# Optimization experiments

Hardware: AMD Instinct MI355X
Metric: run time of the kernel (lower is better)

## Reference

```python
import jax, jax.numpy as jnp
import numpy as np

D_MODEL = 1024
D_STATE = 128
HEADDIM = 64
EXPAND = 2
CHUNK = 64
D_CONV = 4
D_INNER = EXPAND * D_MODEL          # 2048
NHEADS = D_INNER // HEADDIM         # 32
D_IN_PROJ = 2 * D_INNER + 2 * D_STATE + NHEADS  # 4384
CONV_CH = D_INNER + 2 * D_STATE     # 2304
EPS = 1e-5


def segsum(x):
    # x: (..., T) -> (..., T, T); out[i, j] = sum_{k=j+1..i} x[k] for i>=j else -inf
    T = x.shape[-1]
    m1 = jnp.tril(jnp.ones((T, T), bool), -1)
    xr = jnp.where(m1, x[..., :, None], 0.0)   # zero above/at diagonal before cumsum
    s = jnp.cumsum(xr, axis=-2)
    m0 = jnp.tril(jnp.ones((T, T), bool), 0)
    return jnp.where(m0, s, -jnp.inf)


def ssd(x, A, B, C, chunk):
    # x: (b, L, h, p); A: (b, L, h); B, C: (b, L, n)  (the h=1 dim of the torch code is squeezed)
    b, L, h, p = x.shape
    c = L // chunk
    x = x.reshape(b, c, chunk, h, p)
    A = A.reshape(b, c, chunk, h).transpose(0, 3, 1, 2)  # (b, h, c, l)
    B = B.reshape(b, c, chunk, -1)                       # (b, c, l, n)
    C = C.reshape(b, c, chunk, -1)
    A_cum = jnp.cumsum(A, axis=-1)                       # (b, h, c, l)
    Lm = jnp.exp(segsum(A))                              # (b, h, c, l, l)
    # intra-chunk (diagonal block) output
    Y_diag = jnp.einsum('bcln,bcsn,bhcls,bcshp->bclhp', C, B, Lm, x)
    # per-chunk states
    decay_states = jnp.exp(A_cum[:, :, :, -1:] - A_cum)  # (b, h, c, l)
    states = jnp.einsum('bcln,bhcl,bclhp->bchpn', B, decay_states, x)
    init = jnp.zeros_like(states[:, :1])
    states = jnp.concatenate([init, states], axis=1)     # (b, c+1, h, p, n)
    # inter-chunk recurrence
    Ac_last = jnp.pad(A_cum[:, :, :, -1], ((0, 0), (0, 0), (1, 0)))  # (b, h, c+1)
    decay_chunk = jnp.exp(segsum(Ac_last))               # (b, h, c+1, c+1)
    new_states = jnp.einsum('bhzc,bchpn->bzhpn', decay_chunk, states)
    states = new_states[:, :-1]                          # (b, c, h, p, n)
    sdo = jnp.exp(A_cum)
    Y_off = jnp.einsum('bcln,bchpn,bhcl->bclhp', C, states, sdo)
    return (Y_diag + Y_off).reshape(b, L, h, p)


def setup_inputs() -> dict:
    key = jax.random.key(0)
    ks = jax.random.split(key, 8)
    return {
        'u': jax.random.normal(ks[0], (2, 4096, D_MODEL), jnp.float32),
        'W_in': jax.random.normal(ks[1], (D_MODEL, D_IN_PROJ), jnp.float32) * 0.02,
        'conv_w': jax.random.normal(ks[2], (CONV_CH, D_CONV), jnp.float32) * 0.3,
        'conv_b': jax.random.normal(ks[3], (CONV_CH,), jnp.float32) * 0.1,
        'dt_bias': jax.random.normal(ks[4], (NHEADS,), jnp.float32),
        'A_log': jax.random.normal(ks[5], (NHEADS,), jnp.float32) * 0.5,
        'D': jax.random.normal(ks[6], (NHEADS,), jnp.float32),
        'norm_w': jnp.ones((D_INNER,), jnp.float32),
        'W_out': jax.random.normal(ks[7], (D_INNER, D_MODEL), jnp.float32) * 0.02,
    }


def reference(u, W_in, conv_w, conv_b, dt_bias, A_log, D, norm_w, W_out):
    b, L, _ = u.shape
    zxbcdt = u @ W_in                                    # (b, L, 4384)
    z = zxbcdt[..., :D_INNER]
    xBC = zxbcdt[..., D_INNER:D_INNER + CONV_CH]
    dt = jax.nn.softplus(zxbcdt[..., -NHEADS:] + dt_bias)  # (b, L, h)
    # depthwise causal conv (Conv1d pad=d_conv-1, truncated to L == left-pad only)
    xc = jnp.pad(xBC.transpose(0, 2, 1), ((0, 0), (0, 0), (D_CONV - 1, 0)))
    xc = jax.lax.conv_general_dilated(
        xc, conv_w[:, None, :], (1,), 'VALID',
        feature_group_count=CONV_CH,
        dimension_numbers=('NCH', 'OIH', 'NCH')) + conv_b[None, :, None]
    xBC = jax.nn.silu(xc.transpose(0, 2, 1))             # (b, L, 2304)
    x = xBC[..., :D_INNER].reshape(b, L, NHEADS, HEADDIM)
    B = xBC[..., D_INNER:D_INNER + D_STATE]
    C = xBC[..., D_INNER + D_STATE:]
    A = -jnp.exp(A_log)                                  # (h,)
    y = ssd(x * dt[..., None], A * dt, B, C, CHUNK)
    y = y + x * D[:, None]
    y = y.reshape(b, L, D_INNER)
    # RMSNorm with gate z
    y = y * jax.nn.silu(z)
    y = y * jax.lax.rsqrt(jnp.mean(y * y, axis=-1, keepdims=True) + EPS) * norm_w
    return y @ W_out
```

## Files before the change

### kernel.cpp

```cpp
#include <hip/hip_runtime.h>
#include <hip/hip_bf16.h>
#include <math.h>

#define D_MODEL   1024
#define D_STATE   128
#define HEADDIM   64
#define CHUNK     64
#define D_INNER   2048
#define NHEADS    32
#define D_IN_PROJ 4384
#define CONV_CH   2304
#define RCOLS     2336
#define WINT_ROWS 4480
#define BATCH     2
#define SEQ       4096
#define NCHUNK    64
#define ROWS      (BATCH*SEQ)
#define EPS_RMS   1e-5f

typedef __hip_bfloat16 bf16;
typedef __bf16 bf16x8_t __attribute__((ext_vector_type(8)));
typedef float  f32x4_t  __attribute__((ext_vector_type(4)));

__device__ __forceinline__ float siluf_(float x){ return x/(1.f+expf(-x)); }
__device__ __forceinline__ float ldf(const float* p){ return *p; }
__device__ __forceinline__ float ldf(const bf16* p){ return __bfloat162float(*p); }
__device__ __forceinline__ void  stf(float* p, float v){ *p = v; }
__device__ __forceinline__ void  stf(bf16* p, float v){ *p = __float2bfloat16(v); }

__device__ __forceinline__ __bf16 tobf(float v){
    __hip_bfloat16 t = __float2bfloat16(v);
    return *reinterpret_cast<__bf16*>(&t);
}
__device__ __forceinline__ unsigned short bfbits(float v){
    __hip_bfloat16 t = __float2bfloat16(v);
    return *reinterpret_cast<unsigned short*>(&t);
}
__device__ __forceinline__ float bfbits2f(unsigned short u){
    union { unsigned u; float f; } cv; cv.u = ((unsigned)u) << 16; return cv.f;
}

__device__ __forceinline__ void async16(const void* g, void* l) {
    __builtin_amdgcn_global_load_lds(
        (const __attribute__((address_space(1))) unsigned int*)g,
        (__attribute__((address_space(3))) unsigned int*)l, 16, 0, 0);
}

struct GemmCore {
    f32x4_t acc[4][4];
    __device__ __forceinline__ void run(const bf16* __restrict__ A, int lda,
                                        const bf16* __restrict__ Bt, int ldb,
                                        int row0, int col0, int k0, int k1,
                                        __bf16* As, __bf16* Bs,
                                        int wave, int lane) {
        const int quad = lane >> 4, l16 = lane & 15;
        const int wr = (wave >> 1) * 64, wc = (wave & 1) * 64;
#pragma unroll
        for (int i = 0; i < 4; ++i)
#pragma unroll
            for (int j = 0; j < 4; ++j) acc[i][j] = (f32x4_t){0.f, 0.f, 0.f, 0.f};
        const int ca0 = wave * 2, ca1 = wave * 2 + 1;
        const int srow = lane >> 2, scol = (lane & 3) * 8;
        const bf16* Ag0 = A  + (size_t)(row0 + ca0 * 16 + srow) * lda + scol;
        const bf16* Ag1 = A  + (size_t)(row0 + ca1 * 16 + srow) * lda + scol;
        const bf16* Bg0 = Bt + (size_t)(col0 + ca0 * 16 + srow) * ldb + scol;
        const bf16* Bg1 = Bt + (size_t)(col0 + ca1 * 16 + srow) * ldb + scol;
        __bf16* Al0 = As + ca0 * 512;
        __bf16* Al1 = As + ca1 * 512;
        __bf16* Bl0 = Bs + ca0 * 512;
        __bf16* Bl1 = Bs + ca1 * 512;
        for (int kk = k0; kk < k1; kk += 32) {
            async16(Ag0 + kk, Al0);
            async16(Ag1 + kk, Al1);
            async16(Bg0 + kk, Bl0);
            async16(Bg1 + kk, Bl1);
            __syncthreads();
            bf16x8_t af[4], bfr[4];
#pragma unroll
            for (int mi = 0; mi < 4; ++mi)
                af[mi] = *(const bf16x8_t*)(As + (wr + mi * 16 + l16) * 32 + quad * 8);
#pragma unroll
            for (int ni = 0; ni < 4; ++ni)
                bfr[ni] = *(const bf16x8_t*)(Bs + (wc + ni * 16 + l16) * 32 + quad * 8);
#pragma unroll
            for (int mi = 0; mi < 4; ++mi)
#pragma unroll
                for (int ni = 0; ni < 4; ++ni)
                    acc[mi][ni] = __builtin_amdgcn_mfma_f32_16x16x32_bf16(
                        af[mi], bfr[ni], acc[mi][ni], 0, 0, 0);
            __syncthreads();
        }
    }
};

__global__ __launch_bounds__(256) void gemm_zr_fused(const bf16* __restrict__ A,
                                                     const bf16* __restrict__ Bt,
                                                     bf16* __restrict__ Z,
                                                     bf16* __restrict__ R) {
    __shared__ __align__(16) __bf16 As[128 * 32];
    __shared__ __align__(16) __bf16 Bs[128 * 32];
    const int tid = threadIdx.x, wave = tid >> 6, lane = tid & 63;
    const int quad = lane >> 4, l16 = lane & 15;
    const int row0 = blockIdx.x * 128;
    const int ct   = blockIdx.y;
    GemmCore g;
    g.run(A, D_MODEL, Bt, D_MODEL, row0, ct * 128, 0, D_MODEL, As, Bs, wave, lane);

    bf16* Cp; int ldc_, cl0, ncols;
    if (ct < 16) { Cp = Z; ldc_ = D_INNER; cl0 = ct * 128;          ncols = D_INNER; }
    else         { Cp = R; ldc_ = RCOLS;   cl0 = ct * 128 - D_INNER; ncols = RCOLS; }
    const int wr = (wave >> 1) * 64, wc = (wave & 1) * 64;
#pragma unroll
    for (int ni = 0; ni < 4; ++ni) {
        int gc = cl0 + wc + ni * 16 + l16;
        if (gc >= ncols) continue;
#pragma unroll
        for (int mi = 0; mi < 4; ++mi)
#pragma unroll
            for (int r = 0; r < 4; ++r) {
                int gr = row0 + wr + mi * 16 + quad * 4 + r;
                stf(&Cp[(size_t)gr * ldc_ + gc], g.acc[mi][ni][r]);
            }
    }
}

__global__ __launch_bounds__(256) void gemm_out_kernel(const bf16* __restrict__ A,
                                                       const bf16* __restrict__ Bt,
                                                       float* __restrict__ out) {
    __shared__ __align__(16) __bf16 As[128 * 32];
    __shared__ __align__(16) __bf16 Bs[128 * 32];
    const int tid = threadIdx.x, wave = tid >> 6, lane = tid & 63;
    const int quad = lane >> 4, l16 = lane & 15;
    const int row0 = blockIdx.x * 128;
    const int col0 = blockIdx.y * 128;
    GemmCore g;
    g.run(A, D_INNER, Bt, D_INNER, row0, col0, 0, D_INNER, As, Bs, wave, lane);
    const int wr = (wave >> 1) * 64, wc = (wave & 1) * 64;
#pragma unroll
    for (int ni = 0; ni < 4; ++ni) {
        int gc = col0 + wc + ni * 16 + l16;
#pragma unroll
        for (int mi = 0; mi < 4; ++mi)
#pragma unroll
            for (int r = 0; r < 4; ++r) {
                int gr = row0 + wr + mi * 16 + quad * 4 + r;
                out[(size_t)gr * D_MODEL + gc] = g.acc[mi][ni][r];
            }
    }
}

__global__ void cvt_bf16_kernel(const float* __restrict__ src,
                                bf16* __restrict__ dst, int n4) {
    int i = blockIdx.x * 256 + threadIdx.x;
    if (i >= n4) return;
    float4 v = ((const float4*)src)[i];
    dst[i * 4 + 0] = __float2bfloat16(v.x);
    dst[i * 4 + 1] = __float2bfloat16(v.y);
    dst[i * 4 + 2] = __float2bfloat16(v.z);
    dst[i * 4 + 3] = __float2bfloat16(v.w);
}

__global__ __launch_bounds__(256) void transpose_cvt_kernel(const float* __restrict__ W,
                                                            bf16* __restrict__ Wt,
                                                            int R, int C, int Cpad) {
    __shared__ float tile[32][33];
    int c0 = blockIdx.x * 32, r0 = blockIdx.y * 32;
    int tx = threadIdx.x & 31, ty = threadIdx.x >> 5;
    for (int i = ty; i < 32; i += 8) {
        int r = r0 + i, c = c0 + tx;
        tile[i][tx] = (c < C) ? W[(size_t)r * C + c] : 0.f;
    }
    __syncthreads();
    for (int i = ty; i < 32; i += 8) {
        int c = c0 + i, r = r0 + tx;
        stf(&Wt[(size_t)c * R + r], tile[tx][i]);
    }
}

__global__ void prep_convw_kernel(const float* __restrict__ conv_w,
                                  bf16* __restrict__ Wc) {
    int i = blockIdx.x * 256 + threadIdx.x;
    if (i >= CONV_CH * 4) return;
    int ch = i >> 2, k = i & 3;
    Wc[k * CONV_CH + ch] = __float2bfloat16(conv_w[ch * 4 + k]);
}

__global__ __launch_bounds__(256) void conv_silu_kernel(const bf16* __restrict__ R,
                                                        const bf16* __restrict__ Wc,
                                                        const float* __restrict__ conv_b,
                                                        bf16* __restrict__ xBC) {
    int idx = blockIdx.x * 256 + threadIdx.x;
    int rq = idx / 288;
    int g = idx - rq * 288;
    int ch0 = g * 8;
    int row0 = rq * 4;
    int l0 = row0 & (SEQ - 1);

    uint4 rv[7];
#pragma unroll
    for (int j = 0; j < 7; ++j) {
        int ls = l0 - 3 + j;
        rv[j] = (ls >= 0) ? *(const uint4*)&R[(size_t)(row0 - 3 + j) * RCOLS + ch0]
                          : make_uint4(0u, 0u, 0u, 0u);
    }
    uint4 wv[4];
#pragma unroll
    for (int k = 0; k < 4; ++k)
        wv[k] = *(const uint4*)&Wc[k * CONV_CH + ch0];
    float4 b0 = ((const float4*)conv_b)[ch0 / 4];
    float4 b1 = ((const float4*)conv_b)[ch0 / 4 + 1];
    const float bias[8] = {b0.x, b0.y, b0.z, b0.w, b1.x, b1.y, b1.z, b1.w};
    float wf[4][8];
#pragma unroll
    for (int k = 0; k < 4; ++k) {
        const unsigned* wp = (const unsigned*)&wv[k];
#pragma unroll
        for (int j2 = 0; j2 < 4; ++j2) {
            wf[k][2 * j2]     = bfbits2f((unsigned short)(wp[j2] & 0xffff));
            wf[k][2 * j2 + 1] = bfbits2f((unsigned short)(wp[j2] >> 16));
        }
    }
#pragma unroll
    for (int j = 0; j < 4; ++j) {
        float acc[8];
#pragma unroll
        for (int cc = 0; cc < 8; ++cc) acc[cc] = bias[cc];
#pragma unroll
        for (int k = 0; k < 4; ++k) {
            const unsigned* vp = (const unsigned*)&rv[j + k];
#pragma unroll
            for (int j2 = 0; j2 < 4; ++j2) {
                unsigned v = vp[j2];
                acc[2 * j2]     += wf[k][2 * j2]     * bfbits2f((unsigned short)(v & 0xffff));
                acc[2 * j2 + 1] += wf[k][2 * j2 + 1] * bfbits2f((unsigned short)(v >> 16));
            }
        }
        unsigned o[4];
#pragma unroll
        for (int j2 = 0; j2 < 4; ++j2)
            o[j2] = (unsigned)bfbits(siluf_(acc[2 * j2])) |
                    ((unsigned)bfbits(siluf_(acc[2 * j2 + 1])) << 16);
        *(uint4*)&xBC[(size_t)(row0 + j) * CONV_CH + ch0] = make_uint4(o[0], o[1], o[2], o[3]);
    }
}

__global__ void dt_kernel(const bf16* __restrict__ R,
                          const float* __restrict__ dt_bias,
                          float* __restrict__ dtb) {
    int i = blockIdx.x * 256 + threadIdx.x;
    int row = i >> 2, h0 = (i & 3) * 8;
    uint4 v = *(const uint4*)&R[(size_t)row * RCOLS + CONV_CH + h0];
    float4 bia0 = ((const float4*)dt_bias)[h0 / 4];
    float4 bia1 = ((const float4*)dt_bias)[h0 / 4 + 1];
    const unsigned vv[4] = {v.x, v.y, v.z, v.w};
    const float bb[8] = {bia0.x, bia0.y, bia0.z, bia0.w, bia1.x, bia1.y, bia1.z, bia1.w};
    float o[8];
#pragma unroll
    for (int j = 0; j < 4; ++j) {
        float a = bfbits2f((unsigned short)(vv[j] & 0xffff)) + bb[2*j];
        float c = bfbits2f((unsigned short)(vv[j] >> 16)) + bb[2*j+1];
        o[2*j]   = (a > 20.f) ? a : log1pf(expf(a));
        o[2*j+1] = (c > 20.f) ? c : log1pf(expf(c));
    }
    float* dp = &dtb[(size_t)row * NHEADS + h0];
    *(float4*)dp       = make_float4(o[0], o[1], o[2], o[3]);
    *(float4*)(dp + 4) = make_float4(o[4], o[5], o[6], o[7]);
}

__global__ void acum_kernel(const float* __restrict__ dtb,
                            const float* __restrict__ A_log,
                            float* __restrict__ Acum) {
    int bch = blockIdx.x;
    int h = bch & 31;
    int bc = bch >> 5;
    int c = bc & 63, b = bc >> 6;
    int row0 = b * SEQ + c * CHUNK;
    __shared__ float sh[64];
    int l = threadIdx.x;
    float Ah = -expf(A_log[h]);
    sh[l] = Ah * dtb[(size_t)(row0 + l) * NHEADS + h];
    __syncthreads();
    float s = 0.f;
    for (int j = 0; j <= l; ++j) s += sh[j];
    Acum[(size_t)bch * 64 + l] = s;
}

__global__ __launch_bounds__(256) void states_mfma_kernel(const bf16* __restrict__ xBC,
                                                          const float* __restrict__ dtb,
                                                          const float* __restrict__ Acum,
                                                          bf16* __restrict__ states) {
    __shared__ __align__(16) __bf16 BsT[128 * 72];
    __shared__ __align__(16) __bf16 xdT[4][64 * 72];
    __shared__ float dtdec[4][64];
    int bcq = blockIdx.x;
    int hq = bcq & 7, bc = bcq >> 3;
    int c = bc & 63, b = bc >> 6;
    int tid = threadIdx.x, wave = tid >> 6, lane = tid & 63;
    int h = hq * 4 + wave;
    int bch = bc * 32 + h;
    int row0 = b * SEQ + c * CHUNK;
    int quad = lane >> 4, l16 = lane & 15;

    {
        float alast = Acum[(size_t)bch * 64 + 63];
        float a = Acum[(size_t)bch * 64 + lane];
        dtdec[wave][lane] = dtb[(size_t)(row0 + lane) * NHEADS + h] * expf(alast - a);
    }
    __syncthreads();
    for (int it = 0; it < 16; ++it) {
        int i2 = tid + 256 * it;
        int l = i2 >> 6;
        int n0 = (i2 & 63) * 2;
        unsigned v = *(const unsigned*)&xBC[(size_t)(row0 + l) * CONV_CH + D_INNER + n0];
        *(unsigned short*)&BsT[(n0    ) * 72 + l] = (unsigned short)(v & 0xffff);
        *(unsigned short*)&BsT[(n0 + 1) * 72 + l] = (unsigned short)(v >> 16);
    }
    for (int it = 0; it < 32; ++it) {
        int l = 2 * it + (lane >> 5);
        int p0 = (lane & 31) * 2;
        unsigned v = *(const unsigned*)&xBC[(size_t)(row0 + l) * CONV_CH + h * 64 + p0];
        float f = dtdec[wave][l];
        xdT[wave][(p0    ) * 72 + l] = tobf(bfbits2f((unsigned short)(v & 0xffff)) * f);
        xdT[wave][(p0 + 1) * 72 + l] = tobf(bfbits2f((unsigned short)(v >> 16)) * f);
    }
    __syncthreads();

    f32x4_t acc[4][8];
#pragma unroll
    for (int i = 0; i < 4; ++i)
#pragma unroll
        for (int j = 0; j < 8; ++j) acc[i][j] = (f32x4_t){0.f, 0.f, 0.f, 0.f};
#pragma unroll
    for (int ks = 0; ks < 2; ++ks) {
        bf16x8_t a[4], bb[8];
#pragma unroll
        for (int mi = 0; mi < 4; ++mi)
            a[mi] = *(const bf16x8_t*)(&xdT[wave][(mi * 16 + l16) * 72 + ks * 32 + quad * 8]);
#pragma unroll
        for (int ni = 0; ni < 8; ++ni)
            bb[ni] = *(const bf16x8_t*)(&BsT[(ni * 16 + l16) * 72 + ks * 32 + quad * 8]);
#pragma unroll
        for (int mi = 0; mi < 4; ++mi)
#pragma unroll
            for (int ni = 0; ni < 8; ++ni)
                acc[mi][ni] = __builtin_amdgcn_mfma_f32_16x16x32_bf16(
                    a[mi], bb[ni], acc[mi][ni], 0, 0, 0);
    }
#pragma unroll
    for (int ni = 0; ni < 8; ++ni) {
        int n = ni * 16 + l16;
#pragma unroll
        for (int mi = 0; mi < 4; ++mi)
#pragma unroll
            for (int r = 0; r < 4; ++r) {
                int p = mi * 16 + quad * 4 + r;
                stf(&states[(size_t)bch * 8192 + p * 128 + n], acc[mi][ni][r]);
            }
    }
}

__global__ void scan_kernel(const float* __restrict__ Acum,
                            bf16* __restrict__ states) {
    int i = blockIdx.x * 256 + threadIdx.x;
    int pn0 = (i & 2047) * 4;
    int bh = i >> 11;
    int h = bh & 31, b = bh >> 5;
    float carry[4] = {0.f, 0.f, 0.f, 0.f};
    for (int c = 0; c < NCHUNK; ++c) {
        int bch = (b * NCHUNK + c) * NHEADS + h;
        bf16* sp = &states[(size_t)bch * 8192 + pn0];
        uint2 v = *(const uint2*)sp;
        float s0 = bfbits2f((unsigned short)(v.x & 0xffff));
        float s1 = bfbits2f((unsigned short)(v.x >> 16));
        float s2 = bfbits2f((unsigned short)(v.y & 0xffff));
        float s3 = bfbits2f((unsigned short)(v.y >> 16));
        uint2 o;
        o.x = (unsigned)bfbits(carry[0]) | ((unsigned)bfbits(carry[1]) << 16);
        o.y = (unsigned)bfbits(carry[2]) | ((unsigned)bfbits(carry[3]) << 16);
        *(uint2*)sp = o;
        float dec = expf(Acum[(size_t)bch * 64 + 63]);
        carry[0] = carry[0] * dec + s0;
        carry[1] = carry[1] * dec + s1;
        carry[2] = carry[2] * dec + s2;
        carry[3] = carry[3] * dec + s3;
    }
}

__global__ __launch_bounds__(64) void y_mfma_kernel(const bf16* __restrict__ xBC,
                                                    const float* __restrict__ dtb,
                                                    const float* __restrict__ Acum,
                                                    const bf16* __restrict__ states,
                                                    const float* __restrict__ Dv,
                                                    bf16* __restrict__ y) {
    __shared__ __align__(16) __bf16 Mm[64 * 72];
    __shared__ __align__(16) __bf16 xsT[64 * 72];
    __shared__ float acs[64], dtss[64], sdos[64];
    int bch = blockIdx.x;
    int h = bch & 31, bc = bch >> 5;
    int c = bc & 63, b = bc >> 6;
    int row0 = b * SEQ + c * CHUNK;
    int lane = threadIdx.x;
    int quad = lane >> 4, l16 = lane & 15;

    {
        float a = Acum[(size_t)bch * 64 + lane];
        acs[lane] = a;
        sdos[lane] = expf(a);
        dtss[lane] = dtb[(size_t)(row0 + lane) * NHEADS + h];
    }
    for (int it = 0; it < 32; ++it) {
        int l = 2 * it + (lane >> 5);
        int p0 = (lane & 31) * 2;
        unsigned v = *(const unsigned*)&xBC[(size_t)(row0 + l) * CONV_CH + h * 64 + p0];
        *(unsigned short*)&xsT[(p0    ) * 72 + l] = (unsigned short)(v & 0xffff);
        *(unsigned short*)&xsT[(p0 + 1) * 72 + l] = (unsigned short)(v >> 16);
    }
    __syncthreads();

    f32x4_t gacc[4][4];
#pragma unroll
    for (int i = 0; i < 4; ++i)
#pragma unroll
        for (int j = 0; j < 4; ++j) gacc[i][j] = (f32x4_t){0.f, 0.f, 0.f, 0.f};
#pragma unroll
    for (int ks = 0; ks < 4; ++ks) {
        bf16x8_t a[4], bb[4];
#pragma unroll
        for (int mi = 0; mi < 4; ++mi)
            a[mi] = *(const bf16x8_t*)&xBC[(size_t)(row0 + mi * 16 + l16) * CONV_CH +
                                           D_INNER + D_STATE + ks * 32 + quad * 8];
#pragma unroll
        for (int ni = 0; ni < 4; ++ni)
            bb[ni] = *(const bf16x8_t*)&xBC[(size_t)(row0 + ni * 16 + l16) * CONV_CH +
                                            D_INNER + ks * 32 + quad * 8];
#pragma unroll
        for (int mi = 0; mi < 4; ++mi)
#pragma unroll
            for (int ni = 0; ni <= mi; ++ni)
                gacc[mi][ni] = __builtin_amdgcn_mfma_f32_16x16x32_bf16(
                    a[mi], bb[ni], gacc[mi][ni], 0, 0, 0);
    }
#pragma unroll
    for (int ni = 0; ni < 4; ++ni) {
        int s = ni * 16 + l16;
        float ds = dtss[s], as = acs[s];
#pragma unroll
        for (int mi = 0; mi < 4; ++mi)
#pragma unroll
            for (int r = 0; r < 4; ++r) {
                int l = mi * 16 + quad * 4 + r;
                float coef = (s <= l) ? gacc[mi][ni][r] * ds * expf(acs[l] - as) : 0.f;
                Mm[l * 72 + s] = tobf(coef);
            }
    }
    __syncthreads();

    f32x4_t acc[4][4];
#pragma unroll
    for (int i = 0; i < 4; ++i)
#pragma unroll
        for (int j = 0; j < 4; ++j) acc[i][j] = (f32x4_t){0.f, 0.f, 0.f, 0.f};

#pragma unroll
    for (int ks = 0; ks < 2; ++ks) {
        bf16x8_t a[4], bb[4];
#pragma unroll
        for (int mi = 0; mi < 4; ++mi)
            a[mi] = *(const bf16x8_t*)(&Mm[(mi * 16 + l16) * 72 + ks * 32 + quad * 8]);
#pragma unroll
        for (int ni = 0; ni < 4; ++ni)
            bb[ni] = *(const bf16x8_t*)(&xsT[(ni * 16 + l16) * 72 + ks * 32 + quad * 8]);
#pragma unroll
        for (int mi = 0; mi < 4; ++mi)
#pragma unroll
            for (int ni = 0; ni < 4; ++ni)
                acc[mi][ni] = __builtin_amdgcn_mfma_f32_16x16x32_bf16(
                    a[mi], bb[ni], acc[mi][ni], 0, 0, 0);
    }
    float sdo_mi[4];
#pragma unroll
    for (int mi = 0; mi < 4; ++mi) sdo_mi[mi] = sdos[mi * 16 + l16];
#pragma unroll
    for (int ks = 0; ks < 4; ++ks) {
        bf16x8_t a[4], bb[4];
#pragma unroll
        for (int mi = 0; mi < 4; ++mi) {
            const unsigned* cp = (const unsigned*)&xBC[(size_t)(row0 + mi * 16 + l16) * CONV_CH
                                                       + D_INNER + D_STATE + ks * 32 + quad * 8];
            float sc = sdo_mi[mi];
#pragma unroll
            for (int jj = 0; jj < 4; ++jj) {
                unsigned v = cp[jj];
                a[mi][2 * jj    ] = tobf(bfbits2f((unsigned short)(v & 0xffff)) * sc);
                a[mi][2 * jj + 1] = tobf(bfbits2f((unsigned short)(v >> 16)) * sc);
            }
        }
#pragma unroll
        for (int ni = 0; ni < 4; ++ni)
            bb[ni] = *(const bf16x8_t*)&states[(size_t)bch * 8192 + (ni * 16 + l16) * 128
                                               + ks * 32 + quad * 8];
#pragma unroll
        for (int mi = 0; mi < 4; ++mi)
#pragma unroll
            for (int ni = 0; ni < 4; ++ni)
                acc[mi][ni] = __builtin_amdgcn_mfma_f32_16x16x32_bf16(
                    a[mi], bb[ni], acc[mi][ni], 0, 0, 0);
    }
    float Dh = Dv[h];
#pragma unroll
    for (int ni = 0; ni < 4; ++ni) {
        int p = ni * 16 + l16;
#pragma unroll
        for (int mi = 0; mi < 4; ++mi)
#pragma unroll
            for (int r = 0; r < 4; ++r) {
                int l = mi * 16 + quad * 4 + r;
                float xv = bfbits2f(*(const unsigned short*)&xsT[p * 72 + l]);
                stf(&y[(size_t)(row0 + l) * D_INNER + h * 64 + p],
                    acc[mi][ni][r] + Dh * xv);
            }
    }
}

__global__ __launch_bounds__(256) void gate_norm_kernel(const bf16* __restrict__ Z,
                                                        const float* __restrict__ nw,
                                                        bf16* __restrict__ y) {
    int row = blockIdx.x;
    int tid = threadIdx.x;
    int col0 = tid * 8;
    uint4 zv = *(const uint4*)&Z[(size_t)row * D_INNER + col0];
    uint4 yv = *(const uint4*)&y[(size_t)row * D_INNER + col0];
    const unsigned zz[4] = {zv.x, zv.y, zv.z, zv.w};
    const unsigned yy[4] = {yv.x, yv.y, yv.z, yv.w};
    float vals[8];
    float local = 0.f;
#pragma unroll
    for (int j = 0; j < 4; ++j) {
        float z0 = bfbits2f((unsigned short)(zz[j] & 0xffff));
        float z1 = bfbits2f((unsigned short)(zz[j] >> 16));
        float y0 = bfbits2f((unsigned short)(yy[j] & 0xffff));
        float y1 = bfbits2f((unsigned short)(yy[j] >> 16));
        float v0 = y0 * siluf_(z0);
        float v1 = y1 * siluf_(z1);
        vals[2*j] = v0; vals[2*j+1] = v1;
        local += v0 * v0 + v1 * v1;
    }
#pragma unroll
    for (int off = 32; off; off >>= 1) local += __shfl_down(local, off, 64);
    __shared__ float wsum[4];
    if ((tid & 63) == 0) wsum[tid >> 6] = local;
    __syncthreads();
    float total = wsum[0] + wsum[1] + wsum[2] + wsum[3];
    float scale = rsqrtf(total / (float)D_INNER + EPS_RMS);
    float4 w0 = ((const float4*)nw)[col0 / 4];
    float4 w1 = ((const float4*)nw)[col0 / 4 + 1];
    const float ww[8] = {w0.x, w0.y, w0.z, w0.w, w1.x, w1.y, w1.z, w1.w};
    unsigned o[4];
#pragma unroll
    for (int j = 0; j < 4; ++j)
        o[j] = (unsigned)bfbits(vals[2*j] * scale * ww[2*j]) |
               ((unsigned)bfbits(vals[2*j+1] * scale * ww[2*j+1]) << 16);
    *(uint4*)&y[(size_t)row * D_INNER + col0] = make_uint4(o[0], o[1], o[2], o[3]);
}

extern "C" void kernel_launch(void* const* d_in, const int* in_sizes, int n_in,
                              void* d_out, int out_size, void* d_ws, size_t ws_size,
                              hipStream_t stream) {
    const float* u       = (const float*)d_in[0];
    const float* W_in    = (const float*)d_in[1];
    const float* conv_w  = (const float*)d_in[2];
    const float* conv_b  = (const float*)d_in[3];
    const float* dt_bias = (const float*)d_in[4];
    const float* A_log   = (const float*)d_in[5];
    const float* Dv      = (const float*)d_in[6];
    const float* norm_w  = (const float*)d_in[7];
    const float* W_out   = (const float*)d_in[8];
    float* out = (float*)d_out;

    const size_t sz_xBC    = (size_t)ROWS * CONV_CH * 2;
    const size_t sz_Z      = (size_t)ROWS * D_INNER * 2;
    const size_t sz_y      = (size_t)ROWS * D_INNER * 2;
    const size_t sz_states = (size_t)BATCH * NCHUNK * NHEADS * 8192 * 2;
    const size_t sz_dtb    = (size_t)ROWS * NHEADS * 4;
    const size_t sz_Acum   = (size_t)BATCH * NCHUNK * NHEADS * 64 * 4;
    const size_t sz_WinT   = (size_t)WINT_ROWS * D_MODEL * 2;
    const size_t sz_WoutT  = (size_t)D_MODEL * D_INNER * 2;
    const size_t sz_Wc     = (size_t)CONV_CH * 4 * 2;
    const size_t need = sz_xBC + sz_Z + sz_y + sz_states + sz_dtb + sz_Acum +
                        sz_WinT + sz_WoutT + sz_Wc;
    if (ws_size < need) {
        hipMemsetAsync(d_out, 0, (size_t)out_size * sizeof(float), stream);
        return;
    }
    char* ws = (char*)d_ws;
    size_t off = 0;
    bf16*  xBC    = (bf16*) (ws + off); off += sz_xBC;
    bf16*  Z      = (bf16*) (ws + off); off += sz_Z;
    bf16*  y      = (bf16*) (ws + off); off += sz_y;
    bf16*  states = (bf16*) (ws + off); off += sz_states;
    float* dtb    = (float*)(ws + off); off += sz_dtb;
    float* Acum   = (float*)(ws + off); off += sz_Acum;
    bf16*  W_inT  = (bf16*) (ws + off); off += sz_WinT;
    bf16*  W_outT = (bf16*) (ws + off); off += sz_WoutT;
    bf16*  Wc     = (bf16*) (ws + off); off += sz_Wc;
    bf16*  R        = states;
    bf16*  u_bf16   = (bf16*)((char*)states + (size_t)ROWS * RCOLS * 2);

    cvt_bf16_kernel<<<(ROWS * D_MODEL / 4 + 255) / 256, 256, 0, stream>>>(
        u, u_bf16, ROWS * D_MODEL / 4);
    transpose_cvt_kernel<<<dim3(WINT_ROWS / 32, D_MODEL / 32), 256, 0, stream>>>(
        W_in, W_inT, D_MODEL, D_IN_PROJ, WINT_ROWS);
    transpose_cvt_kernel<<<dim3(D_MODEL / 32, D_INNER / 32), 256, 0, stream>>>(
        W_out, W_outT, D_INNER, D_MODEL, D_MODEL);
    prep_convw_kernel<<<(CONV_CH * 4 + 255) / 256, 256, 0, stream>>>(conv_w, Wc);
    gemm_zr_fused<<<dim3(ROWS / 128, 35), 256, 0, stream>>>(u_bf16, W_inT, Z, R);
    conv_silu_kernel<<<ROWS / 4 * 288 / 256, 256, 0, stream>>>(R, Wc, conv_b, xBC);
    dt_kernel<<<ROWS * 4 / 256, 256, 0, stream>>>(R, dt_bias, dtb);
    acum_kernel<<<BATCH * NCHUNK * NHEADS, 64, 0, stream>>>(dtb, A_log, Acum);
    states_mfma_kernel<<<BATCH * NCHUNK * 8, 256, 0, stream>>>(xBC, dtb, Acum, states);
    scan_kernel<<<BATCH * NHEADS * 2048 / 256, 256, 0, stream>>>(Acum, states);
    y_mfma_kernel<<<BATCH * NCHUNK * NHEADS, 64, 0, stream>>>(
        xBC, dtb, Acum, states, Dv, y);
    gate_norm_kernel<<<ROWS, 256, 0, stream>>>(Z, norm_w, y);
    gemm_out_kernel<<<dim3(ROWS / 128, D_MODEL / 128), 256, 0, stream>>>(
        y, W_outT, out);
}
```

Measured before the change: 415.0 us.

## Fuse prep kernels, precompute chunk decays, prefetch scan loads, pack LDS transposes

Measured after the change: 411.5 us. About the same (-0.8%).

```diff
diff --git a/kernel.cpp b/kernel.cpp
--- a/kernel.cpp
+++ b/kernel.cpp
@@ -23,8 +23,6 @@
 typedef float  f32x4_t  __attribute__((ext_vector_type(4)));
 
 __device__ __forceinline__ float siluf_(float x){ return x/(1.f+expf(-x)); }
-__device__ __forceinline__ float ldf(const float* p){ return *p; }
-__device__ __forceinline__ float ldf(const bf16* p){ return __bfloat162float(*p); }
 __device__ __forceinline__ void  stf(float* p, float v){ *p = v; }
 __device__ __forceinline__ void  stf(bf16* p, float v){ *p = __float2bfloat16(v); }
 
@@ -149,40 +147,58 @@
     }
 }
 
-__global__ void cvt_bf16_kernel(const float* __restrict__ src,
-                                bf16* __restrict__ dst, int n4) {
-    int i = blockIdx.x * 256 + threadIdx.x;
-    if (i >= n4) return;
-    float4 v = ((const float4*)src)[i];
-    dst[i * 4 + 0] = __float2bfloat16(v.x);
-    dst[i * 4 + 1] = __float2bfloat16(v.y);
-    dst[i * 4 + 2] = __float2bfloat16(v.z);
-    dst[i * 4 + 3] = __float2bfloat16(v.w);
-}
-
-__global__ __launch_bounds__(256) void transpose_cvt_kernel(const float* __restrict__ W,
-                                                            bf16* __restrict__ Wt,
-                                                            int R, int C, int Cpad) {
+__global__ __launch_bounds__(256) void prep_all_kernel(const float* __restrict__ u,
+                                                       bf16* __restrict__ u_bf16,
+                                                       const float* __restrict__ W_in,
+                                                       bf16* __restrict__ W_inT,
+                                                       const float* __restrict__ W_out,
+                                                       bf16* __restrict__ W_outT,
+                                                       const float* __restrict__ conv_w,
+                                                       bf16* __restrict__ Wc) {
     __shared__ float tile[32][33];
-    int c0 = blockIdx.x * 32, r0 = blockIdx.y * 32;
-    int tx = threadIdx.x & 31, ty = threadIdx.x >> 5;
-    for (int i = ty; i < 32; i += 8) {
-        int r = r0 + i, c = c0 + tx;
-        tile[i][tx] = (c < C) ? W[(size_t)r * C + c] : 0.f;
-    }
-    __syncthreads();
-    for (int i = ty; i < 32; i += 8) {
-        int c = c0 + i, r = r0 + tx;
-        stf(&Wt[(size_t)c * R + r], tile[tx][i]);
-    }
-}
-
-__global__ void prep_convw_kernel(const float* __restrict__ conv_w,
-                                  bf16* __restrict__ Wc) {
-    int i = blockIdx.x * 256 + threadIdx.x;
-    if (i >= CONV_CH * 4) return;
-    int ch = i >> 2, k = i & 3;
-    Wc[k * CONV_CH + ch] = __float2bfloat16(conv_w[ch * 4 + k]);
+    int bid = blockIdx.x;
+    const int tid = threadIdx.x;
+
+    auto do_transpose = [&](const float* W, bf16* Wt, int R, int C, int c0, int r0) {
+        int tx = tid & 31, ty = tid >> 5;
+        for (int i = ty; i < 32; i += 8) {
+            int r = r0 + i, c = c0 + tx;
+            tile[i][tx] = (c < C) ? W[(size_t)r * C + c] : 0.f;
+        }
+        __syncthreads();
+        for (int i = ty; i < 32; i += 8) {
+            int c = c0 + i, r = r0 + tx;
+            stf(&Wt[(size_t)c * R + r], tile[tx][i]);
+        }
+    };
+
+    if (bid < 8192) {
+        int i = bid * 256 + tid;
+        float4 v = ((const float4*)u)[i];
+        u_bf16[i * 4 + 0] = __float2bfloat16(v.x);
+        u_bf16[i * 4 + 1] = __float2bfloat16(v.y);
+        u_bf16[i * 4 + 2] = __float2bfloat16(v.z);
+        u_bf16[i * 4 + 3] = __float2bfloat16(v.w);
+        return;
+    }
+    bid -= 8192;
+    if (bid < (WINT_ROWS / 32) * (D_MODEL / 32)) {
+        int bx = bid % (WINT_ROWS / 32), by = bid / (WINT_ROWS / 32);
+        do_transpose(W_in, W_inT, D_MODEL, D_IN_PROJ, bx * 32, by * 32);
+        return;
+    }
+    bid -= (WINT_ROWS / 32) * (D_MODEL / 32);
+    if (bid < (D_MODEL / 32) * (D_INNER / 32)) {
+        int bx = bid % (D_MODEL / 32), by = bid / (D_MODEL / 32);
+        do_transpose(W_out, W_outT, D_INNER, D_MODEL, bx * 32, by * 32);
+        return;
+    }
+    bid -= (D_MODEL / 32) * (D_INNER / 32);
+    int i = bid * 256 + tid;
+    if (i < CONV_CH * 4) {
+        int ch = i >> 2, k = i & 3;
+        Wc[k * CONV_CH + ch] = __float2bfloat16(conv_w[ch * 4 + k]);
+    }
 }
 
 __global__ __launch_bounds__(256) void conv_silu_kernel(const bf16* __restrict__ R,
@@ -269,7 +285,8 @@
 
 __global__ void acum_kernel(const float* __restrict__ dtb,
                             const float* __restrict__ A_log,
-                            float* __restrict__ Acum) {
+                            float* __restrict__ Acum,
+                            float* __restrict__ decs) {
     int bch = blockIdx.x;
     int h = bch & 31;
     int bc = bch >> 5;
@@ -283,6 +300,7 @@
     float s = 0.f;
     for (int j = 0; j <= l; ++j) s += sh[j];
     Acum[(size_t)bch * 64 + l] = s;
+    if (l == 63) decs[bch] = expf(s);
 }
 
 __global__ __launch_bounds__(256) void states_mfma_kernel(const bf16* __restrict__ xBC,
@@ -307,21 +325,27 @@
         dtdec[wave][lane] = dtb[(size_t)(row0 + lane) * NHEADS + h] * expf(alast - a);
     }
     __syncthreads();
+    for (int it = 0; it < 8; ++it) {
+        int i2 = tid + 256 * it;
+        int l0 = (i2 >> 6) * 2;
+        int n0 = (i2 & 63) * 2;
+        unsigned v0 = *(const unsigned*)&xBC[(size_t)(row0 + l0    ) * CONV_CH + D_INNER + n0];
+        unsigned v1 = *(const unsigned*)&xBC[(size_t)(row0 + l0 + 1) * CONV_CH + D_INNER + n0];
+        *(unsigned*)&BsT[(n0    ) * 72 + l0] = (v0 & 0xffffu) | (v1 << 16);
+        *(unsigned*)&BsT[(n0 + 1) * 72 + l0] = (v0 >> 16) | (v1 & 0xffff0000u);
+    }
     for (int it = 0; it < 16; ++it) {
-        int i2 = tid + 256 * it;
-        int l = i2 >> 6;
-        int n0 = (i2 & 63) * 2;
-        unsigned v = *(const unsigned*)&xBC[(size_t)(row0 + l) * CONV_CH + D_INNER + n0];
-        *(unsigned short*)&BsT[(n0    ) * 72 + l] = (unsigned short)(v & 0xffff);
-        *(unsigned short*)&BsT[(n0 + 1) * 72 + l] = (unsigned short)(v >> 16);
-    }
-    for (int it = 0; it < 32; ++it) {
-        int l = 2 * it + (lane >> 5);
+        int l0 = 4 * it + ((lane >> 5) << 1);
         int p0 = (lane & 31) * 2;
-        unsigned v = *(const unsigned*)&xBC[(size_t)(row0 + l) * CONV_CH + h * 64 + p0];
-        float f = dtdec[wave][l];
-        xdT[wave][(p0    ) * 72 + l] = tobf(bfbits2f((unsigned short)(v & 0xffff)) * f);
-        xdT[wave][(p0 + 1) * 72 + l] = tobf(bfbits2f((unsigned short)(v >> 16)) * f);
+        unsigned v0 = *(const unsigned*)&xBC[(size_t)(row0 + l0    ) * CONV_CH + h * 64 + p0];
+        unsigned v1 = *(const unsigned*)&xBC[(size_t)(row0 + l0 + 1) * CONV_CH + h * 64 + p0];
+        float f0 = dtdec[wave][l0], f1 = dtdec[wave][l0 + 1];
+        unsigned w0 = (unsigned)bfbits(bfbits2f((unsigned short)(v0 & 0xffff)) * f0)
+                    | ((unsigned)bfbits(bfbits2f((unsigned short)(v1 & 0xffff)) * f1) << 16);
+        unsigned w1 = (unsigned)bfbits(bfbits2f((unsigned short)(v0 >> 16)) * f0)
+                    | ((unsigned)bfbits(bfbits2f((unsigned short)(v1 >> 16)) * f1) << 16);
+        *(unsigned*)&xdT[wave][(p0    ) * 72 + l0] = w0;
+        *(unsigned*)&xdT[wave][(p0 + 1) * 72 + l0] = w1;
     }
     __syncthreads();
 
@@ -359,30 +383,30 @@
     }
 }
 
-__global__ void scan_kernel(const float* __restrict__ Acum,
+__global__ void scan_kernel(const float* __restrict__ decs,
                             bf16* __restrict__ states) {
     int i = blockIdx.x * 256 + threadIdx.x;
     int pn0 = (i & 2047) * 4;
     int bh = i >> 11;
     int h = bh & 31, b = bh >> 5;
+    int bch0 = b * NCHUNK * NHEADS + h;
+    const size_t cstride = (size_t)NHEADS * 8192;
     float carry[4] = {0.f, 0.f, 0.f, 0.f};
+    bf16* sp = &states[(size_t)bch0 * 8192 + pn0];
+    uint2 v = *(const uint2*)sp;
     for (int c = 0; c < NCHUNK; ++c) {
-        int bch = (b * NCHUNK + c) * NHEADS + h;
-        bf16* sp = &states[(size_t)bch * 8192 + pn0];
-        uint2 v = *(const uint2*)sp;
-        float s0 = bfbits2f((unsigned short)(v.x & 0xffff));
-        float s1 = bfbits2f((unsigned short)(v.x >> 16));
-        float s2 = bfbits2f((unsigned short)(v.y & 0xffff));
-        float s3 = bfbits2f((unsigned short)(v.y >> 16));
+        bf16* spn = sp + ((c + 1 < NCHUNK) ? cstride : 0);
+        uint2 vn = *(const uint2*)spn;
+        float dec = decs[bch0 + c * NHEADS];
         uint2 o;
         o.x = (unsigned)bfbits(carry[0]) | ((unsigned)bfbits(carry[1]) << 16);
         o.y = (unsigned)bfbits(carry[2]) | ((unsigned)bfbits(carry[3]) << 16);
         *(uint2*)sp = o;
-        float dec = expf(Acum[(size_t)bch * 64 + 63]);
-        carry[0] = carry[0] * dec + s0;
-        carry[1] = carry[1] * dec + s1;
-        carry[2] = carry[2] * dec + s2;
-        carry[3] = carry[3] * dec + s3;
+        carry[0] = carry[0] * dec + bfbits2f((unsigned short)(v.x & 0xffff));
+        carry[1] = carry[1] * dec + bfbits2f((unsigned short)(v.x >> 16));
+        carry[2] = carry[2] * dec + bfbits2f((unsigned short)(v.y & 0xffff));
+        carry[3] = carry[3] * dec + bfbits2f((unsigned short)(v.y >> 16));
+        sp = spn; v = vn;
     }
 }
 
@@ -408,12 +432,13 @@
         sdos[lane] = expf(a);
         dtss[lane] = dtb[(size_t)(row0 + lane) * NHEADS + h];
     }
-    for (int it = 0; it < 32; ++it) {
-        int l = 2 * it + (lane >> 5);
+    for (int it = 0; it < 16; ++it) {
+        int l0 = 4 * it + ((lane >> 5) << 1);
         int p0 = (lane & 31) * 2;
-        unsigned v = *(const unsigned*)&xBC[(size_t)(row0 + l) * CONV_CH + h * 64 + p0];
-        *(unsigned short*)&xsT[(p0    ) * 72 + l] = (unsigned short)(v & 0xffff);
-        *(unsigned short*)&xsT[(p0 + 1) * 72 + l] = (unsigned short)(v >> 16);
+        unsigned v0 = *(const unsigned*)&xBC[(size_t)(row0 + l0    ) * CONV_CH + h * 64 + p0];
+        unsigned v1 = *(const unsigned*)&xBC[(size_t)(row0 + l0 + 1) * CONV_CH + h * 64 + p0];
+        *(unsigned*)&xsT[(p0    ) * 72 + l0] = (v0 & 0xffffu) | (v1 << 16);
+        *(unsigned*)&xsT[(p0 + 1) * 72 + l0] = (v0 >> 16) | (v1 & 0xffff0000u);
     }
     __syncthreads();
 
@@ -583,11 +608,12 @@
     const size_t sz_states = (size_t)BATCH * NCHUNK * NHEADS * 8192 * 2;
     const size_t sz_dtb    = (size_t)ROWS * NHEADS * 4;
     const size_t sz_Acum   = (size_t)BATCH * NCHUNK * NHEADS * 64 * 4;
+    const size_t sz_decs   = (size_t)BATCH * NCHUNK * NHEADS * 4;
     const size_t sz_WinT   = (size_t)WINT_ROWS * D_MODEL * 2;
     const size_t sz_WoutT  = (size_t)D_MODEL * D_INNER * 2;
     const size_t sz_Wc     = (size_t)CONV_CH * 4 * 2;
     const size_t need = sz_xBC + sz_Z + sz_y + sz_states + sz_dtb + sz_Acum +
-                        sz_WinT + sz_WoutT + sz_Wc;
+                        sz_decs + sz_WinT + sz_WoutT + sz_Wc;
     if (ws_size < need) {
         hipMemsetAsync(d_out, 0, (size_t)out_size * sizeof(float), stream);
         return;
@@ -600,25 +626,23 @@
     bf16*  states = (bf16*) (ws + off); off += sz_states;
     float* dtb    = (float*)(ws + off); off += sz_dtb;
     float* Acum   = (float*)(ws + off); off += sz_Acum;
+    float* decs   = (float*)(ws + off); off += sz_decs;
     bf16*  W_inT  = (bf16*) (ws + off); off += sz_WinT;
     bf16*  W_outT = (bf16*) (ws + off); off += sz_WoutT;
     bf16*  Wc     = (bf16*) (ws + off); off += sz_Wc;
     bf16*  R        = states;
     bf16*  u_bf16   = (bf16*)((char*)states + (size_t)ROWS * RCOLS * 2);
 
-    cvt_bf16_kernel<<<(ROWS * D_MODEL / 4 + 255) / 256, 256, 0, stream>>>(
-        u, u_bf16, ROWS * D_MODEL / 4);
-    transpose_cvt_kernel<<<dim3(WINT_ROWS / 32, D_MODEL / 32), 256, 0, stream>>>(
-        W_in, W_inT, D_MODEL, D_IN_PROJ, WINT_ROWS);
-    transpose_cvt_kernel<<<dim3(D_MODEL / 32, D_INNER / 32), 256, 0, stream>>>(
-        W_out, W_outT, D_INNER, D_MODEL, D_MODEL);
-    prep_convw_kernel<<<(CONV_CH * 4 + 255) / 256, 256, 0, stream>>>(conv_w, Wc);
+    const int prep_blocks = 8192 + (WINT_ROWS / 32) * (D_MODEL / 32)
+                          + (D_MODEL / 32) * (D_INNER / 32) + 36;
+    prep_all_kernel<<<prep_blocks, 256, 0, stream>>>(
+        u, u_bf16, W_in, W_inT, W_out, W_outT, conv_w, Wc);
     gemm_zr_fused<<<dim3(ROWS / 128, 35), 256, 0, stream>>>(u_bf16, W_inT, Z, R);
     conv_silu_kernel<<<ROWS / 4 * 288 / 256, 256, 0, stream>>>(R, Wc, conv_b, xBC);
     dt_kernel<<<ROWS * 4 / 256, 256, 0, stream>>>(R, dt_bias, dtb);
-    acum_kernel<<<BATCH * NCHUNK * NHEADS, 64, 0, stream>>>(dtb, A_log, Acum);
+    acum_kernel<<<BATCH * NCHUNK * NHEADS, 64, 0, stream>>>(dtb, A_log, Acum, decs);
     states_mfma_kernel<<<BATCH * NCHUNK * 8, 256, 0, stream>>>(xBC, dtb, Acum, states);
-    scan_kernel<<<BATCH * NHEADS * 2048 / 256, 256, 0, stream>>>(Acum, states);
+    scan_kernel<<<BATCH * NHEADS * 2048 / 256, 256, 0, stream>>>(decs, states);
     y_mfma_kernel<<<BATCH * NCHUNK * NHEADS, 64, 0, stream>>>(
         xBC, dtb, Acum, states, Dv, y);
     gate_norm_kernel<<<ROWS, 256, 0, stream>>>(Z, norm_w, y);
```
